# Optimization experiments

Measured on AMD Instinct MI355X. Metric: run time of the kernel, lower is better.

## Reference

```python
import math
import jax
import jax.numpy as jnp
import numpy as np

WH, WW = 8, 8
DIM, NUM_HEADS = 768, 24
CPB_HIDDEN = 512


def _rel_tables(Wh, Ww):
    # relative_position_index: (N, N) int, values in [0, (2Wh-1)*(2Ww-1))
    coords = np.stack(np.meshgrid(np.arange(Wh), np.arange(Ww), indexing='ij')).reshape(2, -1)
    rel = coords[:, :, None] - coords[:, None, :]          # (2, N, N)
    rel = rel.transpose(1, 2, 0).astype(np.int64)          # (N, N, 2)
    rel[:, :, 0] += Wh - 1
    rel[:, :, 1] += Ww - 1
    rel[:, :, 0] *= 2 * Ww - 1
    idx = rel.sum(-1)                                      # (N, N)
    # relative_coords_table: ((2Wh-1)*(2Ww-1), 2), log-spaced CPB coords
    rch = np.arange(-(Wh - 1), Wh, dtype=np.float32)
    rcw = np.arange(-(Ww - 1), Ww, dtype=np.float32)
    table = np.stack(np.meshgrid(rch, rcw, indexing='ij')).transpose(1, 2, 0).reshape(-1, 2)
    table[:, 0] /= max(Wh - 1, 1)
    table[:, 1] /= max(Ww - 1, 1)
    table *= 8.0
    table = np.sign(table) * np.log2(np.abs(table) + 1.0) / math.log2(8.0)
    return idx.astype(np.int32), table.astype(np.float32)


def setup_inputs() -> dict:
    key = jax.random.key(0)
    ks = jax.random.split(key, 8)
    B_, N, C = 1024, WH * WW, DIM
    idx, table = _rel_tables(WH, WW)
    return {
        'x': jax.random.normal(ks[0], (B_, N, C), dtype=jnp.float32),
        'qkv_w': jax.random.normal(ks[1], (C, 3 * C), dtype=jnp.float32) * 0.02,
        'qkv_b': jnp.zeros((3 * C,), dtype=jnp.float32),
        'proj_w': jax.random.normal(ks[2], (C, C), dtype=jnp.float32) * 0.02,
        'proj_b': jnp.zeros((C,), dtype=jnp.float32),
        'cpb_w1': jax.random.normal(ks[3], (2, CPB_HIDDEN), dtype=jnp.float32) * 0.1,
        'cpb_b1': jnp.zeros((CPB_HIDDEN,), dtype=jnp.float32),
        'cpb_w2': jax.random.normal(ks[4], (CPB_HIDDEN, NUM_HEADS), dtype=jnp.float32) * 0.05,
        'logit_scale': jnp.full((NUM_HEADS, 1, 1), math.log(10.0), dtype=jnp.float32),
        'rel_coords_table': jnp.asarray(table),
        'rel_pos_index': jnp.asarray(idx),
    }


def reference(x, qkv_w, qkv_b, proj_w, proj_b, cpb_w1, cpb_b1, cpb_w2,
              logit_scale, rel_coords_table, rel_pos_index):
    B_, N, C = x.shape
    H = logit_scale.shape[0]
    hd = C // H
    qkv = (x @ qkv_w + qkv_b).reshape(B_, N, 3, H, hd).transpose(2, 0, 3, 1, 4)
    q, k, v = qkv[0], qkv[1], qkv[2]                        # (B_, H, N, hd)
    # cosine attention: L2-normalize q, k (eps as in F.normalize)
    q = q / jnp.maximum(jnp.linalg.norm(q, axis=-1, keepdims=True), 1e-12)
    k = k / jnp.maximum(jnp.linalg.norm(k, axis=-1, keepdims=True), 1e-12)
    ls = jnp.exp(jnp.minimum(logit_scale, math.log(1.0 / 0.01)))  # (H,1,1)
    q = q * ls
    # CPB bias: MLP over rel coords table, gather by relative_position_index
    bias_table = jnp.maximum(rel_coords_table @ cpb_w1 + cpb_b1, 0.0) @ cpb_w2  # (T, H)
    bias = bias_table[rel_pos_index.reshape(-1)].reshape(N, N, H).transpose(2, 0, 1)[None]  # (1,H,N,N)
    attn = jnp.einsum('bhnd,bhmd->bhnm', q, k) + bias      # scale = 1.0
    attn = jax.nn.softmax(attn, axis=-1)
    out = jnp.einsum('bhnm,bhmd->bhnd', attn, v)
    out = out.transpose(0, 2, 1, 3).reshape(B_, N, C)
    return out @ proj_w + proj_b
```

## Files before the change

kernel.cpp:

```cpp
#include <hip/hip_runtime.h>
#include <hip/hip_bf16.h>

typedef __bf16 bf16_t;
typedef __bf16 bf16x8 __attribute__((ext_vector_type(8)));
typedef float f32x4 __attribute__((ext_vector_type(4)));

static __device__ __forceinline__ f32x4 mfma16(bf16x8 a, bf16x8 b, f32x4 c) {
  return __builtin_amdgcn_mfma_f32_16x16x32_bf16(a, b, c, 0, 0, 0);
}

static __device__ __forceinline__ void gload16(const void* g, void* l) {
  __builtin_amdgcn_global_load_lds(
      (const __attribute__((address_space(1))) void*)g,
      (__attribute__((address_space(3))) void*)l, 16, 0, 0);
}

#define BAR() __builtin_amdgcn_s_barrier()
#define SCHED0() __builtin_amdgcn_sched_barrier(0)
#define WAITVM2() do { asm volatile("s_waitcnt vmcnt(2)" ::: "memory"); SCHED0(); } while (0)
#define WAITVM0() do { asm volatile("s_waitcnt vmcnt(0)" ::: "memory"); SCHED0(); } while (0)
#define WAITLGKM0() do { asm volatile("s_waitcnt lgkmcnt(0)" ::: "memory"); SCHED0(); } while (0)

__global__ __launch_bounds__(256) void cvt_bf16_kernel(
    const float* __restrict__ in, bf16_t* __restrict__ out, int n8) {
  int i = blockIdx.x * 256 + threadIdx.x;
  int stride = gridDim.x * 256;
  for (; i < n8; i += stride) {
    float4 a = ((const float4*)in)[2 * i];
    float4 b = ((const float4*)in)[2 * i + 1];
    bf16x8 w = {(bf16_t)a.x, (bf16_t)a.y, (bf16_t)a.z, (bf16_t)a.w,
                (bf16_t)b.x, (bf16_t)b.y, (bf16_t)b.z, (bf16_t)b.w};
    ((bf16x8*)out)[i] = w;
  }
}

__global__ __launch_bounds__(256) void transpose_cvt_kernel(
    const float* __restrict__ W, bf16_t* __restrict__ WT, int K, int N) {
  __shared__ float tile[32][33];
  int n0 = blockIdx.x * 32, k0 = blockIdx.y * 32;
  int tx = threadIdx.x & 31, ty = threadIdx.x >> 5;
#pragma unroll
  for (int i = 0; i < 32; i += 8)
    tile[ty + i][tx] = W[(size_t)(k0 + ty + i) * N + n0 + tx];
  __syncthreads();
#pragma unroll
  for (int i = 0; i < 32; i += 8)
    WT[(size_t)(n0 + ty + i) * K + k0 + tx] = (bf16_t)tile[tx][ty + i];
}

__global__ __launch_bounds__(512) void cpb_table_kernel(
    const float* __restrict__ table, const float* __restrict__ w1,
    const float* __restrict__ b1, const float* __restrict__ w2,
    float* __restrict__ bias_table) {
  __shared__ float hbuf[512];
  int t = blockIdx.x;
  int j = threadIdx.x;
  float c0 = table[2 * t], c1 = table[2 * t + 1];
  float h = c0 * w1[j] + c1 * w1[512 + j] + b1[j];
  hbuf[j] = h > 0.f ? h : 0.f;
  __syncthreads();
  int wave = j >> 6, lane = j & 63;
  for (int hh = wave * 3; hh < wave * 3 + 3; ++hh) {
    float s = 0.f;
    for (int jj = lane; jj < 512; jj += 64) s += hbuf[jj] * w2[jj * 24 + hh];
    for (int off = 32; off > 0; off >>= 1) s += __shfl_down(s, off, 64);
    if (lane == 0) bias_table[t * 24 + hh] = s;
  }
}

__global__ __launch_bounds__(256) void bias_expand_kernel(
    const float* __restrict__ bias_table, const int* __restrict__ idx,
    float* __restrict__ bias) {
  int h = blockIdx.x;
  for (int nm = threadIdx.x; nm < 4096; nm += 256)
    bias[h * 4096 + nm] = bias_table[idx[nm] * 24 + h];
}

#define MFMA_QUAD(MRLO)                                          \
  do {                                                           \
    _Pragma("unroll") for (int mr = 0; mr < 4; ++mr)             \
        _Pragma("unroll") for (int nc = 0; nc < 4; ++nc)         \
            acc[MRLO + mr][nc] =                                 \
        mfma16(af[MRLO + mr], bfr[nc], acc[MRLO + mr][nc]);      \
  } while (0)

template <int EPI, int NCOLS, int K>
__global__ __launch_bounds__(512, 2) void gemm_kernel(
    const bf16_t* __restrict__ A, const bf16_t* __restrict__ BT,
    const float* __restrict__ bias, void* __restrict__ outp) {
  constexpr int NT = NCOLS / 256;
  constexpr int Kb = K * 2;
  constexpr int nk = K / 32;
  __shared__ __align__(16) char lds[65536];
  int tid = threadIdx.x;
  int wave = tid >> 6, lane = tid & 63;
  int wm = wave >> 2, wn = wave & 3;
  int cpx = gridDim.x >> 3;
  int wg = (blockIdx.x & 7) * cpx + (blockIdx.x >> 3);
  int mt = wg / NT, nt = wg % NT;
  int m0 = mt * 256, n0 = nt * 256;

  int wST = ((tid & 63) * 16);
  wST ^= (((wST >> 9) & 1) << 5);
  int srow = ((tid >> 6) << 4) + (wST >> 6);
  int scolb = wST & 63;
  const char* Asrc = (const char*)A + (size_t)(m0 + srow) * Kb + scolb;
  const char* Bsrc = (const char*)BT + (size_t)(n0 + srow) * Kb + scolb;
  char* Adst = lds + tid * 16;
  char* Bdst = lds + 32768 + tid * 16;

  int rr = lane & 15;
  int wRD = (rr * 64 + ((lane >> 4) * 16)) ^ (((rr >> 3) & 1) << 5);
  const char* aRd = lds + wm * 8192 + wRD;
  const char* bRd = lds + 32768 + (wn >> 1) * 8192 + (wn & 1) * 4096 + wRD;

#define STAGE_A(BUF, H, KT) \
  gload16(Asrc + (size_t)(H)*128 * Kb + (size_t)(KT)*64, Adst + ((BUF) << 14) + ((H) << 13))
#define STAGE_B(BUF, H, KT) \
  gload16(Bsrc + (size_t)(H)*128 * Kb + (size_t)(KT)*64, Bdst + ((BUF) << 14) + ((H) << 13))

  f32x4 acc[8][4] = {};
  STAGE_A(0, 0, 0); STAGE_A(0, 1, 0);
  STAGE_B(0, 0, 0); STAGE_B(0, 1, 0);
  STAGE_A(1, 0, 1); STAGE_A(1, 1, 1);
  WAITVM2();
  BAR(); SCHED0();

  for (int t = 0; t < nk; ++t) {
    int buf = t & 1;
    int bufo = buf << 14;
    if (t + 1 < nk) { STAGE_B(buf ^ 1, 0, t + 1); STAGE_B(buf ^ 1, 1, t + 1); }
    bf16x8 af[8], bfr[4];
#pragma unroll
    for (int mr = 0; mr < 8; ++mr)
      af[mr] = *(const bf16x8*)(aRd + bufo + mr * 1024);
#pragma unroll
    for (int nc = 0; nc < 4; ++nc)
      bfr[nc] = *(const bf16x8*)(bRd + bufo + nc * 1024);
    BAR(); SCHED0();
    __builtin_amdgcn_s_setprio(1);
    MFMA_QUAD(0);
    __builtin_amdgcn_s_setprio(0);
    WAITLGKM0();
    BAR(); SCHED0();
    if (t + 2 < nk) { STAGE_A(buf, 0, t + 2); STAGE_A(buf, 1, t + 2); }
    __builtin_amdgcn_s_setprio(1);
    MFMA_QUAD(4);
    __builtin_amdgcn_s_setprio(0);
    if (t + 2 < nk) { WAITVM2(); }
    else if (t + 1 < nk) { WAITVM0(); }
    if (t + 1 < nk) { BAR(); SCHED0(); }
  }

  int hi4 = (lane >> 4) * 4;
  if constexpr (EPI == 0) {
    bf16_t* out = (bf16_t*)outp;
    int sidx = n0 / 768;
#pragma unroll
    for (int mr = 0; mr < 8; ++mr)
#pragma unroll
      for (int nc = 0; nc < 4; ++nc) {
        int gcol = n0 + wn * 64 + nc * 16 + (lane & 15);
        int within = gcol - sidx * 768;
        int h = within >> 5, d = within & 31;
        float bv = bias[gcol];
#pragma unroll
        for (int j = 0; j < 4; ++j) {
          int grow = m0 + wm * 128 + mr * 16 + hi4 + j;
          int bwin = grow >> 6, nn = grow & 63;
          size_t off = ((((size_t)sidx * 1024 + bwin) * 24 + h) * 64 + nn) * 32 + d;
          out[off] = (bf16_t)(acc[mr][nc][j] + bv);
        }
      }
  } else {
    float* out = (float*)outp;
#pragma unroll
    for (int mr = 0; mr < 8; ++mr)
#pragma unroll
      for (int nc = 0; nc < 4; ++nc) {
        int gcol = n0 + wn * 64 + nc * 16 + (lane & 15);
        float bv = bias[gcol];
#pragma unroll
        for (int j = 0; j < 4; ++j) {
          int grow = m0 + wm * 128 + mr * 16 + hi4 + j;
          out[(size_t)grow * NCOLS + gcol] = acc[mr][nc][j] + bv;
        }
      }
  }
}

__global__ __launch_bounds__(64) void attn_kernel(
    const bf16_t* __restrict__ qkv, const float* __restrict__ bias,
    const float* __restrict__ logit_scale, bf16_t* __restrict__ attn_out) {
  __shared__ __align__(16) char smem[14848];
  bf16_t (*qs)[40] = (bf16_t(*)[40])smem;
  bf16_t (*kk)[40] = (bf16_t(*)[40])(smem + 5120);
  bf16_t (*vT)[72] = (bf16_t(*)[72])(smem + 10240);
  bf16_t (*ps)[72] = (bf16_t(*)[72])smem;
  int h = blockIdx.x >> 10;
  int b = blockIdx.x & 1023;
  int lane = threadIdx.x;
  float ls = __expf(fminf(logit_scale[h], 4.6051701859880914f));
  size_t base = ((size_t)b * 24 + h) * 2048;
  const bf16_t* qrow = qkv + base + lane * 32;
  const bf16_t* krow = qkv + (size_t)50331648 + base + lane * 32;
  const bf16_t* vrow = qkv + (size_t)100663296 + base + lane * 32;
  {
    bf16x8 r[4];
#pragma unroll
    for (int i = 0; i < 4; ++i) r[i] = *(const bf16x8*)(qrow + i * 8);
    float f[32], sq = 0.f;
#pragma unroll
    for (int i = 0; i < 4; ++i)
#pragma unroll
      for (int j = 0; j < 8; ++j) { float x = (float)r[i][j]; f[i * 8 + j] = x; sq += x * x; }
    float sc = ls / fmaxf(sqrtf(sq), 1e-12f);
#pragma unroll
    for (int i = 0; i < 4; ++i) {
      bf16x8 w;
#pragma unroll
      for (int j = 0; j < 8; ++j) w[j] = (bf16_t)(f[i * 8 + j] * sc);
      *(bf16x8*)&qs[lane][i * 8] = w;
    }
  }
  {
    bf16x8 r[4];
#pragma unroll
    for (int i = 0; i < 4; ++i) r[i] = *(const bf16x8*)(krow + i * 8);
    float f[32], sq = 0.f;
#pragma unroll
    for (int i = 0; i < 4; ++i)
#pragma unroll
      for (int j = 0; j < 8; ++j) { float x = (float)r[i][j]; f[i * 8 + j] = x; sq += x * x; }
    float sc = 1.f / fmaxf(sqrtf(sq), 1e-12f);
#pragma unroll
    for (int i = 0; i < 4; ++i) {
      bf16x8 w;
#pragma unroll
      for (int j = 0; j < 8; ++j) w[j] = (bf16_t)(f[i * 8 + j] * sc);
      *(bf16x8*)&kk[lane][i * 8] = w;
    }
  }
  {
    bf16x8 r[4];
#pragma unroll
    for (int i = 0; i < 4; ++i) r[i] = *(const bf16x8*)(vrow + i * 8);
#pragma unroll
    for (int i = 0; i < 4; ++i)
#pragma unroll
      for (int j = 0; j < 8; ++j) vT[i * 8 + j][lane] = r[i][j];
  }
  __syncthreads();
  f32x4 sacc[4][4] = {};
  {
    bf16x8 qa[4], kb[4];
#pragma unroll
    for (int mr = 0; mr < 4; ++mr)
      qa[mr] = *(bf16x8*)&qs[mr * 16 + (lane & 15)][(lane >> 4) * 8];
#pragma unroll
    for (int nc = 0; nc < 4; ++nc)
      kb[nc] = *(bf16x8*)&kk[nc * 16 + (lane & 15)][(lane >> 4) * 8];
#pragma unroll
    for (int mr = 0; mr < 4; ++mr)
#pragma unroll
      for (int nc = 0; nc < 4; ++nc)
        sacc[mr][nc] = mfma16(qa[mr], kb[nc], sacc[mr][nc]);
  }
  const float* bh = bias + h * 4096;
  int hi4 = (lane >> 4) * 4;
#pragma unroll
  for (int mr = 0; mr < 4; ++mr)
#pragma unroll
    for (int j = 0; j < 4; ++j) {
      int r = mr * 16 + hi4 + j;
      float v0 = sacc[mr][0][j] + bh[r * 64 + 0 + (lane & 15)];
      float v1 = sacc[mr][1][j] + bh[r * 64 + 16 + (lane & 15)];
      float v2 = sacc[mr][2][j] + bh[r * 64 + 32 + (lane & 15)];
      float v3 = sacc[mr][3][j] + bh[r * 64 + 48 + (lane & 15)];
      float m = fmaxf(fmaxf(v0, v1), fmaxf(v2, v3));
#pragma unroll
      for (int off = 1; off < 16; off <<= 1) m = fmaxf(m, __shfl_xor(m, off, 64));
      v0 = __expf(v0 - m); v1 = __expf(v1 - m);
      v2 = __expf(v2 - m); v3 = __expf(v3 - m);
      float sum = v0 + v1 + v2 + v3;
#pragma unroll
      for (int off = 1; off < 16; off <<= 1) sum += __shfl_xor(sum, off, 64);
      float inv = 1.f / sum;
      ps[r][0 + (lane & 15)] = (bf16_t)(v0 * inv);
      ps[r][16 + (lane & 15)] = (bf16_t)(v1 * inv);
      ps[r][32 + (lane & 15)] = (bf16_t)(v2 * inv);
      ps[r][48 + (lane & 15)] = (bf16_t)(v3 * inv);
    }
  __syncthreads();
  f32x4 oacc[4][2] = {};
#pragma unroll
  for (int ks_ = 0; ks_ < 2; ++ks_) {
    bf16x8 pa[4], vb[2];
#pragma unroll
    for (int mr = 0; mr < 4; ++mr)
      pa[mr] = *(bf16x8*)&ps[mr * 16 + (lane & 15)][ks_ * 32 + (lane >> 4) * 8];
#pragma unroll
    for (int c2 = 0; c2 < 2; ++c2)
      vb[c2] = *(bf16x8*)&vT[c2 * 16 + (lane & 15)][ks_ * 32 + (lane >> 4) * 8];
#pragma unroll
    for (int mr = 0; mr < 4; ++mr)
#pragma unroll
      for (int c2 = 0; c2 < 2; ++c2)
        oacc[mr][c2] = mfma16(pa[mr], vb[c2], oacc[mr][c2]);
  }
#pragma unroll
  for (int mr = 0; mr < 4; ++mr)
#pragma unroll
    for (int c2 = 0; c2 < 2; ++c2) {
      int d = c2 * 16 + (lane & 15);
#pragma unroll
      for (int j = 0; j < 4; ++j) {
        int r = mr * 16 + hi4 + j;
        attn_out[((size_t)b * 64 + r) * 768 + h * 32 + d] = (bf16_t)oacc[mr][c2][j];
      }
    }
}

extern "C" void kernel_launch(void* const* d_in, const int* in_sizes, int n_in,
                              void* d_out, int out_size, void* d_ws, size_t ws_size,
                              hipStream_t stream) {
  const float* x = (const float*)d_in[0];
  const float* qkv_w = (const float*)d_in[1];
  const float* qkv_b = (const float*)d_in[2];
  const float* proj_w = (const float*)d_in[3];
  const float* proj_b = (const float*)d_in[4];
  const float* cpb_w1 = (const float*)d_in[5];
  const float* cpb_b1 = (const float*)d_in[6];
  const float* cpb_w2 = (const float*)d_in[7];
  const float* logit_scale = (const float*)d_in[8];
  const float* rel_tab = (const float*)d_in[9];
  const int* rel_idx = (const int*)d_in[10];

  char* ws = (char*)d_ws;
  float* bias_table = (float*)ws;
  float* bias = (float*)(ws + 32768);
  bf16_t* wTq = (bf16_t*)(ws + 425984);
  bf16_t* wTp = (bf16_t*)(ws + 3964928);
  bf16_t* qkv = (bf16_t*)(ws + 5144576);
  bf16_t* xb = (bf16_t*)(ws + 307134464);
  bf16_t* attn = xb;

  cvt_bf16_kernel<<<2048, 256, 0, stream>>>(x, xb, 6291456);
  transpose_cvt_kernel<<<dim3(72, 24), 256, 0, stream>>>(qkv_w, wTq, 768, 2304);
  transpose_cvt_kernel<<<dim3(24, 24), 256, 0, stream>>>(proj_w, wTp, 768, 768);
  cpb_table_kernel<<<225, 512, 0, stream>>>(rel_tab, cpb_w1, cpb_b1, cpb_w2, bias_table);
  bias_expand_kernel<<<24, 256, 0, stream>>>(bias_table, rel_idx, bias);
  gemm_kernel<0, 2304, 768><<<2304, 512, 0, stream>>>(xb, wTq, qkv_b, qkv);
  attn_kernel<<<24576, 64, 0, stream>>>(qkv, bias, logit_scale, attn);
  gemm_kernel<1, 768, 768><<<768, 512, 0, stream>>>(attn, wTp, proj_b, d_out);
}
```

Measured before the change: 583.9 us.

## Deepen GEMM K-tile to 64 with 128KB LDS and finer-grained interleaved pipeline

```diff
diff --git a/kernel.cpp b/kernel.cpp
--- a/kernel.cpp
+++ b/kernel.cpp
@@ -17,9 +17,13 @@
 
 #define BAR() __builtin_amdgcn_s_barrier()
 #define SCHED0() __builtin_amdgcn_sched_barrier(0)
-#define WAITVM2() do { asm volatile("s_waitcnt vmcnt(2)" ::: "memory"); SCHED0(); } while (0)
+#define MEMFENCE() asm volatile("" ::: "memory")
+#define BARF() do { BAR(); MEMFENCE(); SCHED0(); } while (0)
+#define WAITVM4() do { asm volatile("s_waitcnt vmcnt(4)" ::: "memory"); SCHED0(); } while (0)
 #define WAITVM0() do { asm volatile("s_waitcnt vmcnt(0)" ::: "memory"); SCHED0(); } while (0)
 #define WAITLGKM0() do { asm volatile("s_waitcnt lgkmcnt(0)" ::: "memory"); SCHED0(); } while (0)
+#define SP1 __builtin_amdgcn_s_setprio(1)
+#define SP0 __builtin_amdgcn_s_setprio(0)
 
 __global__ __launch_bounds__(256) void cvt_bf16_kernel(
     const float* __restrict__ in, bf16_t* __restrict__ out, int n8) {
@@ -76,22 +80,15 @@
     bias[h * 4096 + nm] = bias_table[idx[nm] * 24 + h];
 }
 
-#define MFMA_QUAD(MRLO)                                          \
-  do {                                                           \
-    _Pragma("unroll") for (int mr = 0; mr < 4; ++mr)             \
-        _Pragma("unroll") for (int nc = 0; nc < 4; ++nc)         \
-            acc[MRLO + mr][nc] =                                 \
-        mfma16(af[MRLO + mr], bfr[nc], acc[MRLO + mr][nc]);      \
-  } while (0)
-
 template <int EPI, int NCOLS, int K>
 __global__ __launch_bounds__(512, 2) void gemm_kernel(
     const bf16_t* __restrict__ A, const bf16_t* __restrict__ BT,
     const float* __restrict__ bias, void* __restrict__ outp) {
   constexpr int NT = NCOLS / 256;
   constexpr int Kb = K * 2;
-  constexpr int nk = K / 32;
-  __shared__ __align__(16) char lds[65536];
+  constexpr int nk = K / 64;
+  constexpr int nIt = nk / 2;
+  __shared__ __align__(16) char lds[131072];
   int tid = threadIdx.x;
   int wave = tid >> 6, lane = tid & 63;
   int wm = wave >> 2, wn = wave & 3;
@@ -100,56 +97,143 @@
   int mt = wg / NT, nt = wg % NT;
   int m0 = mt * 256, n0 = nt * 256;
 
-  int wST = ((tid & 63) * 16);
-  wST ^= (((wST >> 9) & 1) << 5);
-  int srow = ((tid >> 6) << 4) + (wST >> 6);
-  int scolb = wST & 63;
-  const char* Asrc = (const char*)A + (size_t)(m0 + srow) * Kb + scolb;
-  const char* Bsrc = (const char*)BT + (size_t)(n0 + srow) * Kb + scolb;
-  char* Adst = lds + tid * 16;
-  char* Bdst = lds + 32768 + tid * 16;
-
-  int rr = lane & 15;
-  int wRD = (rr * 64 + ((lane >> 4) * 16)) ^ (((rr >> 3) & 1) << 5);
-  const char* aRd = lds + wm * 8192 + wRD;
-  const char* bRd = lds + 32768 + (wn >> 1) * 8192 + (wn & 1) * 4096 + wRD;
-
-#define STAGE_A(BUF, H, KT) \
-  gload16(Asrc + (size_t)(H)*128 * Kb + (size_t)(KT)*64, Adst + ((BUF) << 14) + ((H) << 13))
-#define STAGE_B(BUF, H, KT) \
-  gload16(Bsrc + (size_t)(H)*128 * Kb + (size_t)(KT)*64, Bdst + ((BUF) << 14) + ((H) << 13))
+  int srow = tid >> 3;
+  int sbc = ((tid & 7) << 4) ^ ((srow & 7) << 4);
+  const char* Ag = (const char*)A + (size_t)(m0 + srow) * Kb + sbc;
+  const char* Bg = (const char*)BT + (size_t)(n0 + srow) * Kb + sbc;
+  char* Al = lds + tid * 16;
+  char* Bl = lds + 65536 + tid * 16;
+
+#define ST_A(B_, H_, KT_)                                                     \
+  do {                                                                        \
+    gload16(Ag + (size_t)((H_) * 128) * Kb + (KT_) * 128,                     \
+            Al + (B_) * 32768 + (H_) * 16384);                                \
+    gload16(Ag + (size_t)((H_) * 128 + 64) * Kb + (KT_) * 128,                \
+            Al + (B_) * 32768 + (H_) * 16384 + 8192);                         \
+  } while (0)
+#define ST_B(B_, H_, KT_)                                                     \
+  do {                                                                        \
+    gload16(Bg + (size_t)((H_) * 128) * Kb + (KT_) * 128,                     \
+            Bl + (B_) * 32768 + (H_) * 16384);                                \
+    gload16(Bg + (size_t)((H_) * 128 + 64) * Kb + (KT_) * 128,                \
+            Bl + (B_) * 32768 + (H_) * 16384 + 8192);                         \
+  } while (0)
+
+  int r15 = lane & 15, hi = lane >> 4;
+  int swz = (lane & 7) << 4;
+  int c0 = (hi << 4) ^ swz;
+  int c1 = (64 | (hi << 4)) ^ swz;
+  const char* aBase = lds + wm * 16384 + r15 * 128;
+  const char* bBase = lds + 65536 + (wn >> 1) * 16384 + (wn & 1) * 8192 + r15 * 128;
+
+#define RD_B8(B_)                                                             \
+  do {                                                                        \
+    _Pragma("unroll") for (int nc = 0; nc < 4; ++nc) {                        \
+      bfr[nc][0] = *(const bf16x8*)(bBase + (B_) * 32768 + nc * 2048 + c0);   \
+      bfr[nc][1] = *(const bf16x8*)(bBase + (B_) * 32768 + nc * 2048 + c1);   \
+    }                                                                         \
+  } while (0)
+#define RD_A4(B_, MRLO, C_)                                                   \
+  do {                                                                        \
+    _Pragma("unroll") for (int m_ = 0; m_ < 4; ++m_)                          \
+        af[m_] = *(const bf16x8*)(aBase + (B_) * 32768 + ((MRLO) + m_) * 2048 + (C_)); \
+  } while (0)
+#define MF16(MRLO, KKI)                                                       \
+  do {                                                                        \
+    _Pragma("unroll") for (int m_ = 0; m_ < 4; ++m_)                          \
+        _Pragma("unroll") for (int nc = 0; nc < 4; ++nc)                      \
+            acc[(MRLO) + m_][nc] =                                            \
+        mfma16(af[m_], bfr[nc][KKI], acc[(MRLO) + m_][nc]);                   \
+  } while (0)
 
   f32x4 acc[8][4] = {};
-  STAGE_A(0, 0, 0); STAGE_A(0, 1, 0);
-  STAGE_B(0, 0, 0); STAGE_B(0, 1, 0);
-  STAGE_A(1, 0, 1); STAGE_A(1, 1, 1);
-  WAITVM2();
-  BAR(); SCHED0();
-
-  for (int t = 0; t < nk; ++t) {
-    int buf = t & 1;
-    int bufo = buf << 14;
-    if (t + 1 < nk) { STAGE_B(buf ^ 1, 0, t + 1); STAGE_B(buf ^ 1, 1, t + 1); }
-    bf16x8 af[8], bfr[4];
-#pragma unroll
-    for (int mr = 0; mr < 8; ++mr)
-      af[mr] = *(const bf16x8*)(aRd + bufo + mr * 1024);
-#pragma unroll
-    for (int nc = 0; nc < 4; ++nc)
-      bfr[nc] = *(const bf16x8*)(bRd + bufo + nc * 1024);
-    BAR(); SCHED0();
-    __builtin_amdgcn_s_setprio(1);
-    MFMA_QUAD(0);
-    __builtin_amdgcn_s_setprio(0);
-    WAITLGKM0();
-    BAR(); SCHED0();
-    if (t + 2 < nk) { STAGE_A(buf, 0, t + 2); STAGE_A(buf, 1, t + 2); }
-    __builtin_amdgcn_s_setprio(1);
-    MFMA_QUAD(4);
-    __builtin_amdgcn_s_setprio(0);
-    if (t + 2 < nk) { WAITVM2(); }
-    else if (t + 1 < nk) { WAITVM0(); }
-    if (t + 1 < nk) { BAR(); SCHED0(); }
+  ST_B(0, 0, 0); ST_B(0, 1, 0);
+  ST_A(0, 0, 0); ST_A(0, 1, 0);
+  ST_B(1, 0, 1); ST_B(1, 1, 1);
+  WAITVM4();
+  BARF();
+
+  for (int it = 0; it < nIt - 1; ++it) {
+    int T = 2 * it;
+    bf16x8 af[4], bfr[4][2];
+    RD_B8(0); RD_A4(0, 0, c0);
+    ST_A(1, 0, T + 1); ST_A(1, 1, T + 1);
+    BAR(); WAITLGKM0();
+    SP1; MF16(0, 0); SP0;
+    BARF();
+    RD_A4(0, 4, c0);
+    ST_B(0, 0, T + 2);
+    BAR(); WAITLGKM0();
+    SP1; MF16(4, 0); SP0;
+    BARF();
+    RD_A4(0, 0, c1);
+    ST_B(0, 1, T + 2);
+    BAR(); WAITLGKM0();
+    SP1; MF16(0, 1); SP0;
+    BARF();
+    RD_A4(0, 4, c1);
+    BAR(); WAITLGKM0();
+    SP1; MF16(4, 1); SP0;
+    WAITVM4();
+    BARF();
+    RD_B8(1); RD_A4(1, 0, c0);
+    ST_A(0, 0, T + 2);
+    BAR(); WAITLGKM0();
+    SP1; MF16(0, 0); SP0;
+    BARF();
+    RD_A4(1, 4, c0);
+    ST_A(0, 1, T + 2);
+    BAR(); WAITLGKM0();
+    SP1; MF16(4, 0); SP0;
+    BARF();
+    RD_A4(1, 0, c1);
+    ST_B(1, 0, T + 3);
+    BAR(); WAITLGKM0();
+    SP1; MF16(0, 1); SP0;
+    BARF();
+    RD_A4(1, 4, c1);
+    ST_B(1, 1, T + 3);
+    BAR(); WAITLGKM0();
+    SP1; MF16(4, 1); SP0;
+    WAITVM4();
+    BARF();
+  }
+  {
+    constexpr int T = nk - 2;
+    bf16x8 af[4], bfr[4][2];
+    RD_B8(0); RD_A4(0, 0, c0);
+    ST_A(1, 0, T + 1); ST_A(1, 1, T + 1);
+    BAR(); WAITLGKM0();
+    SP1; MF16(0, 0); SP0;
+    BARF();
+    RD_A4(0, 4, c0);
+    BAR(); WAITLGKM0();
+    SP1; MF16(4, 0); SP0;
+    BARF();
+    RD_A4(0, 0, c1);
+    BAR(); WAITLGKM0();
+    SP1; MF16(0, 1); SP0;
+    BARF();
+    RD_A4(0, 4, c1);
+    BAR(); WAITLGKM0();
+    SP1; MF16(4, 1); SP0;
+    WAITVM0();
+    BARF();
+    RD_B8(1); RD_A4(1, 0, c0);
+    BAR(); WAITLGKM0();
+    SP1; MF16(0, 0); SP0;
+    BARF();
+    RD_A4(1, 4, c0);
+    BAR(); WAITLGKM0();
+    SP1; MF16(4, 0); SP0;
+    BARF();
+    RD_A4(1, 0, c1);
+    BAR(); WAITLGKM0();
+    SP1; MF16(0, 1); SP0;
+    BARF();
+    RD_A4(1, 4, c1);
+    BAR(); WAITLGKM0();
+    SP1; MF16(4, 1); SP0;
   }
 
   int hi4 = (lane >> 4) * 4;
@@ -160,7 +244,7 @@
     for (int mr = 0; mr < 8; ++mr)
 #pragma unroll
       for (int nc = 0; nc < 4; ++nc) {
-        int gcol = n0 + wn * 64 + nc * 16 + (lane & 15);
+        int gcol = n0 + wn * 64 + nc * 16 + r15;
         int within = gcol - sidx * 768;
         int h = within >> 5, d = within & 31;
         float bv = bias[gcol];
@@ -178,7 +262,7 @@
     for (int mr = 0; mr < 8; ++mr)
 #pragma unroll
       for (int nc = 0; nc < 4; ++nc) {
-        int gcol = n0 + wn * 64 + nc * 16 + (lane & 15);
+        int gcol = n0 + wn * 64 + nc * 16 + r15;
         float bv = bias[gcol];
 #pragma unroll
         for (int j = 0; j < 4; ++j) {
@@ -187,6 +271,11 @@
         }
       }
   }
+#undef ST_A
+#undef ST_B
+#undef RD_B8
+#undef RD_A4
+#undef MF16
 }
 
 __global__ __launch_bounds__(64) void attn_kernel(
```

New measurement: 554.4 us. 1.05x faster.

## Double K-tile depth to 64 with 128KB LDS double-buffered GEMM pipeline

Applied to the files above, without the earlier changes.

```diff
diff --git a/kernel.cpp b/kernel.cpp
--- a/kernel.cpp
+++ b/kernel.cpp
@@ -17,9 +17,13 @@
 
 #define BAR() __builtin_amdgcn_s_barrier()
 #define SCHED0() __builtin_amdgcn_sched_barrier(0)
-#define WAITVM2() do { asm volatile("s_waitcnt vmcnt(2)" ::: "memory"); SCHED0(); } while (0)
+#define MEMFENCE() asm volatile("" ::: "memory")
+#define BARF() do { BAR(); MEMFENCE(); SCHED0(); } while (0)
+#define WAITVM8() do { asm volatile("s_waitcnt vmcnt(8)" ::: "memory"); SCHED0(); } while (0)
 #define WAITVM0() do { asm volatile("s_waitcnt vmcnt(0)" ::: "memory"); SCHED0(); } while (0)
 #define WAITLGKM0() do { asm volatile("s_waitcnt lgkmcnt(0)" ::: "memory"); SCHED0(); } while (0)
+#define SP1 __builtin_amdgcn_s_setprio(1)
+#define SP0 __builtin_amdgcn_s_setprio(0)
 
 __global__ __launch_bounds__(256) void cvt_bf16_kernel(
     const float* __restrict__ in, bf16_t* __restrict__ out, int n8) {
@@ -76,22 +80,14 @@
     bias[h * 4096 + nm] = bias_table[idx[nm] * 24 + h];
 }
 
-#define MFMA_QUAD(MRLO)                                          \
-  do {                                                           \
-    _Pragma("unroll") for (int mr = 0; mr < 4; ++mr)             \
-        _Pragma("unroll") for (int nc = 0; nc < 4; ++nc)         \
-            acc[MRLO + mr][nc] =                                 \
-        mfma16(af[MRLO + mr], bfr[nc], acc[MRLO + mr][nc]);      \
-  } while (0)
-
 template <int EPI, int NCOLS, int K>
 __global__ __launch_bounds__(512, 2) void gemm_kernel(
     const bf16_t* __restrict__ A, const bf16_t* __restrict__ BT,
     const float* __restrict__ bias, void* __restrict__ outp) {
   constexpr int NT = NCOLS / 256;
   constexpr int Kb = K * 2;
-  constexpr int nk = K / 32;
-  __shared__ __align__(16) char lds[65536];
+  constexpr int nk = K / 64;
+  __shared__ __align__(16) char lds[131072];
   int tid = threadIdx.x;
   int wave = tid >> 6, lane = tid & 63;
   int wm = wave >> 2, wn = wave & 3;
@@ -100,59 +96,83 @@
   int mt = wg / NT, nt = wg % NT;
   int m0 = mt * 256, n0 = nt * 256;
 
-  int wST = ((tid & 63) * 16);
-  wST ^= (((wST >> 9) & 1) << 5);
-  int srow = ((tid >> 6) << 4) + (wST >> 6);
-  int scolb = wST & 63;
-  const char* Asrc = (const char*)A + (size_t)(m0 + srow) * Kb + scolb;
-  const char* Bsrc = (const char*)BT + (size_t)(n0 + srow) * Kb + scolb;
-  char* Adst = lds + tid * 16;
-  char* Bdst = lds + 32768 + tid * 16;
-
-  int rr = lane & 15;
-  int wRD = (rr * 64 + ((lane >> 4) * 16)) ^ (((rr >> 3) & 1) << 5);
-  const char* aRd = lds + wm * 8192 + wRD;
-  const char* bRd = lds + 32768 + (wn >> 1) * 8192 + (wn & 1) * 4096 + wRD;
-
-#define STAGE_A(BUF, H, KT) \
-  gload16(Asrc + (size_t)(H)*128 * Kb + (size_t)(KT)*64, Adst + ((BUF) << 14) + ((H) << 13))
-#define STAGE_B(BUF, H, KT) \
-  gload16(Bsrc + (size_t)(H)*128 * Kb + (size_t)(KT)*64, Bdst + ((BUF) << 14) + ((H) << 13))
+  int srow = tid >> 3;
+  int sbc = ((tid & 7) << 4) ^ ((srow & 7) << 4);
+  const char* Ag = (const char*)A + (size_t)(m0 + srow) * Kb + sbc;
+  const char* Bg = (const char*)BT + (size_t)(n0 + srow) * Kb + sbc;
+  char* Al = lds + tid * 16;
+  char* Bl = lds + 65536 + tid * 16;
+
+#define ST_A(B_, H_, KT_)                                                     \
+  do {                                                                        \
+    gload16(Ag + (size_t)((H_) * 128) * Kb + (KT_) * 128,                     \
+            Al + (B_) * 32768 + (H_) * 16384);                                \
+    gload16(Ag + (size_t)((H_) * 128 + 64) * Kb + (KT_) * 128,                \
+            Al + (B_) * 32768 + (H_) * 16384 + 8192);                         \
+  } while (0)
+#define ST_B(B_, H_, KT_)                                                     \
+  do {                                                                        \
+    gload16(Bg + (size_t)((H_) * 128) * Kb + (KT_) * 128,                     \
+            Bl + (B_) * 32768 + (H_) * 16384);                                \
+    gload16(Bg + (size_t)((H_) * 128 + 64) * Kb + (KT_) * 128,                \
+            Bl + (B_) * 32768 + (H_) * 16384 + 8192);                         \
+  } while (0)
+#define STAGE_PAIR(B_, KT_)                                                   \
+  do { ST_A(B_, 0, KT_); ST_A(B_, 1, KT_); ST_B(B_, 0, KT_); ST_B(B_, 1, KT_); } while (0)
+
+  int r15 = lane & 15, hi = lane >> 4;
+  int swz = (lane & 7) << 4;
+  int c0 = (hi << 4) ^ swz;
+  int c1 = (64 | (hi << 4)) ^ swz;
+  const char* aBase = lds + wm * 16384 + r15 * 128;
+  const char* bBase = lds + 65536 + (wn >> 1) * 16384 + (wn & 1) * 8192 + r15 * 128;
+
+#define RD_A8(B_, C_)                                                         \
+  do {                                                                        \
+    _Pragma("unroll") for (int m_ = 0; m_ < 8; ++m_)                          \
+        af[m_] = *(const bf16x8*)(aBase + (B_) * 32768 + m_ * 2048 + (C_));   \
+  } while (0)
+#define RD_B4(B_, C_)                                                         \
+  do {                                                                        \
+    _Pragma("unroll") for (int n_ = 0; n_ < 4; ++n_)                          \
+        bfr[n_] = *(const bf16x8*)(bBase + (B_) * 32768 + n_ * 2048 + (C_));  \
+  } while (0)
+#define MF32()                                                                \
+  do {                                                                        \
+    _Pragma("unroll") for (int m_ = 0; m_ < 8; ++m_)                          \
+        _Pragma("unroll") for (int n_ = 0; n_ < 4; ++n_)                      \
+            acc[m_][n_] = mfma16(af[m_], bfr[n_], acc[m_][n_]);               \
+  } while (0)
 
   f32x4 acc[8][4] = {};
-  STAGE_A(0, 0, 0); STAGE_A(0, 1, 0);
-  STAGE_B(0, 0, 0); STAGE_B(0, 1, 0);
-  STAGE_A(1, 0, 1); STAGE_A(1, 1, 1);
-  WAITVM2();
-  BAR(); SCHED0();
-
-  for (int t = 0; t < nk; ++t) {
-    int buf = t & 1;
-    int bufo = buf << 14;
-    if (t + 1 < nk) { STAGE_B(buf ^ 1, 0, t + 1); STAGE_B(buf ^ 1, 1, t + 1); }
+  STAGE_PAIR(0, 0);
+  STAGE_PAIR(1, 1);
+  WAITVM8();
+  BARF();
+
+  for (int t = 0; t < nk; t += 2) {
     bf16x8 af[8], bfr[4];
-#pragma unroll
-    for (int mr = 0; mr < 8; ++mr)
-      af[mr] = *(const bf16x8*)(aRd + bufo + mr * 1024);
-#pragma unroll
-    for (int nc = 0; nc < 4; ++nc)
-      bfr[nc] = *(const bf16x8*)(bRd + bufo + nc * 1024);
-    BAR(); SCHED0();
-    __builtin_amdgcn_s_setprio(1);
-    MFMA_QUAD(0);
-    __builtin_amdgcn_s_setprio(0);
-    WAITLGKM0();
-    BAR(); SCHED0();
-    if (t + 2 < nk) { STAGE_A(buf, 0, t + 2); STAGE_A(buf, 1, t + 2); }
-    __builtin_amdgcn_s_setprio(1);
-    MFMA_QUAD(4);
-    __builtin_amdgcn_s_setprio(0);
-    if (t + 2 < nk) { WAITVM2(); }
-    else if (t + 1 < nk) { WAITVM0(); }
-    if (t + 1 < nk) { BAR(); SCHED0(); }
-  }
-
-  int hi4 = (lane >> 4) * 4;
+    RD_A8(0, c0); RD_B4(0, c0);
+    WAITLGKM0(); BAR(); SCHED0();
+    SP1; MF32(); SP0;
+    RD_A8(0, c1); RD_B4(0, c1);
+    WAITLGKM0(); BAR(); SCHED0();
+    SP1; MF32(); SP0;
+    WAITVM0();
+    BARF();
+    RD_A8(1, c0); RD_B4(1, c0);
+    WAITLGKM0(); BAR(); SCHED0();
+    if (t + 2 < nk) STAGE_PAIR(0, t + 2);
+    SP1; MF32(); SP0;
+    RD_A8(1, c1); RD_B4(1, c1);
+    WAITLGKM0(); BAR(); SCHED0();
+    if (t + 3 < nk) STAGE_PAIR(1, t + 3);
+    SP1; MF32(); SP0;
+    if (t + 2 < nk) { WAITVM8(); }
+    BARF();
+  }
+
+  int hi4 = hi * 4;
   if constexpr (EPI == 0) {
     bf16_t* out = (bf16_t*)outp;
     int sidx = n0 / 768;
@@ -160,7 +180,7 @@
     for (int mr = 0; mr < 8; ++mr)
 #pragma unroll
       for (int nc = 0; nc < 4; ++nc) {
-        int gcol = n0 + wn * 64 + nc * 16 + (lane & 15);
+        int gcol = n0 + wn * 64 + nc * 16 + r15;
         int within = gcol - sidx * 768;
         int h = within >> 5, d = within & 31;
         float bv = bias[gcol];
@@ -178,7 +198,7 @@
     for (int mr = 0; mr < 8; ++mr)
 #pragma unroll
       for (int nc = 0; nc < 4; ++nc) {
-        int gcol = n0 + wn * 64 + nc * 16 + (lane & 15);
+        int gcol = n0 + wn * 64 + nc * 16 + r15;
         float bv = bias[gcol];
 #pragma unroll
         for (int j = 0; j < 4; ++j) {
@@ -187,6 +207,12 @@
         }
       }
   }
+#undef ST_A
+#undef ST_B
+#undef STAGE_PAIR
+#undef RD_A8
+#undef RD_B4
+#undef MF32
 }
 
 __global__ __launch_bounds__(64) void attn_kernel(
```

New measurement: 595.9 us. 2.0% more time.
